# Performance work log

Hardware: AMD Instinct MI355X
Metric: run time of the kernel (lower is better)

## Reference

```python
import jax, jax.numpy as jnp
import numpy as np

B, N, H, K = 2, 4096, 256, 24
IN_DIM = 2 * H + 3  # hidden*2 + 3*num_frames


def setup_inputs() -> dict:
    key = jax.random.key(0)
    ks = jax.random.split(key, 8)
    return {
        "p": jax.random.normal(ks[0], (B, N, 3), jnp.float32),
        "R": jax.random.normal(ks[1], (B, N, 3, 3), jnp.float32),
        "h": jax.random.normal(ks[2], (B, N, H), jnp.float32),
        "W1": jax.random.normal(ks[3], (IN_DIM, H), jnp.float32) * (1.0 / np.sqrt(IN_DIM)),
        "b1": jnp.zeros((H,), jnp.float32),
        "W2": jax.random.normal(ks[4], (H, H), jnp.float32) * (1.0 / np.sqrt(H)),
        "b2": jnp.zeros((H,), jnp.float32),
        "W3": jax.random.normal(ks[5], (H, H), jnp.float32) * (1.0 / np.sqrt(H)),
        "b3": jnp.zeros((H,), jnp.float32),
    }


def _knn_idx(x, k):
    # squared euclidean distances (B,N,N); nearest-k (includes self), like knn_points
    sq = jnp.sum(x * x, axis=-1)
    d = sq[:, :, None] + sq[:, None, :] - 2.0 * jnp.einsum("bnd,bmd->bnm", x, x)
    _, idx = jax.lax.top_k(-d, k)  # (B,N,K)
    return idx


def _gather(x, idx):
    # x: (B,N,D), idx: (B,N,K) -> (B,N,K,D)
    return jax.vmap(lambda a, i: a[i])(x, idx)


def reference(p, R, h, W1, b1, W2, b2, W3, b3):
    leaky = lambda x: jax.nn.leaky_relu(x, 0.1)
    idx = _knn_idx(h, K)                     # graph_type='hidden'
    p_j = _gather(p, idx)                    # (B,N,K,3)
    diff = p_j - p[:, :, None, :]            # global offset
    p_ij = jnp.einsum("bnji,bnkj->bnki", R, diff)  # local frame: R^T (p_j - p_i)
    h_j = _gather(h, idx)                    # (B,N,K,H)
    h_i = jnp.broadcast_to(h[:, :, None, :], h_j.shape)
    feat = jnp.concatenate([p_ij, h_i, h_j], axis=-1)  # (B,N,K,515)
    x = leaky(feat @ W1 + b1)
    x = leaky(x @ W2 + b2)
    x = x @ W3 + b3                          # (B,N,K,H)
    return jnp.max(x, axis=2)                # aggr='max' -> (B,N,H)
```

## Files before the change

### kernel.cpp

```cpp
#include <hip/hip_runtime.h>
#include <stdint.h>

#define BATCH 2
#define NPTS  4096
#define HDIM  256
#define KNN   24
#define NEDGE (BATCH * NPTS * KNN)
#define CAP   256
#define TGT   40

typedef __attribute__((ext_vector_type(8))) short bf16x8;
typedef __attribute__((ext_vector_type(4))) float f32x4;

__device__ __forceinline__ unsigned short f2bf(float f) {
  union { float f; unsigned int u; } x; x.f = f;
  unsigned int u = x.u;
  unsigned int r = (u + 0x7fffu + ((u >> 16) & 1u)) >> 16;
  return (unsigned short)r;
}

__device__ __forceinline__ void gl2lds16(const void* g, void* l) {
  __builtin_amdgcn_global_load_lds(
      (const __attribute__((address_space(1))) unsigned int*)g,
      (__attribute__((address_space(3))) unsigned int*)l, 16, 0, 0);
}

__global__ __launch_bounds__(256) void k_sqnorm(const float* __restrict__ h,
                                                float* __restrict__ sq,
                                                unsigned short* __restrict__ hb) {
  int t = threadIdx.x, lane = t & 63, w = t >> 6;
  int row = blockIdx.x * 4 + w;
  const float* hr = h + (size_t)row * HDIM;
  float4 v = *(const float4*)(hr + lane * 4);
  ushort4 o;
  o.x = f2bf(v.x); o.y = f2bf(v.y); o.z = f2bf(v.z); o.w = f2bf(v.w);
  *(ushort4*)(hb + (size_t)row * HDIM + lane * 4) = o;
  float s = v.x * v.x + v.y * v.y + v.z * v.z + v.w * v.w;
#pragma unroll
  for (int off = 32; off; off >>= 1) s += __shfl_down(s, off);
  if (lane == 0) sq[row] = s;
}

__global__ __launch_bounds__(256) void k_convw(const float* __restrict__ W2,
                                               const float* __restrict__ W3,
                                               unsigned short* __restrict__ w2bt,
                                               unsigned short* __restrict__ w3bt) {
  int t = blockIdx.x * 256 + threadIdx.x;
  int k = t >> 8, n = t & 255;
  w2bt[n * 256 + k] = f2bf(W2[t]);
  w3bt[n * 256 + k] = f2bf(W3[t]);
}

__global__ __launch_bounds__(256) void k_dist(const unsigned short* __restrict__ hb,
                                              const float* __restrict__ sq,
                                              float* __restrict__ D) {
  __shared__ unsigned short At[128 * 32];
  __shared__ unsigned short Bl[128 * 32];
  int b = blockIdx.z;
  int i0 = blockIdx.y * 128, j0 = blockIdx.x * 128;
  const unsigned short* A = hb + (size_t)b * NPTS * HDIM;
  int t = threadIdx.x, lane = t & 63, w = t >> 6;
  int wm = w >> 1, wn = w & 1;
  int lr = lane & 15, lk = (lane >> 4) * 8;
  f32x4 acc[4][4];
#pragma unroll
  for (int i = 0; i < 4; ++i)
#pragma unroll
    for (int j = 0; j < 4; ++j) acc[i][j] = (f32x4){0.f, 0.f, 0.f, 0.f};

  for (int k0 = 0; k0 < HDIM; k0 += 32) {
#pragma unroll
    for (int c = 0; c < 2; ++c) {
      int o = c * 256 + t;
      int row = o >> 2, cb = (o & 3) * 16;
      gl2lds16((const char*)A + ((size_t)(i0 + row) * HDIM + k0) * 2 + cb, (char*)At + o * 16);
      gl2lds16((const char*)A + ((size_t)(j0 + row) * HDIM + k0) * 2 + cb, (char*)Bl + o * 16);
    }
    __syncthreads();
    bf16x8 af[4], bfr[4];
#pragma unroll
    for (int i = 0; i < 4; ++i) af[i] = *(const bf16x8*)&At[(wm * 64 + i * 16 + lr) * 32 + lk];
#pragma unroll
    for (int j = 0; j < 4; ++j) bfr[j] = *(const bf16x8*)&Bl[(wn * 64 + j * 16 + lr) * 32 + lk];
#pragma unroll
    for (int i = 0; i < 4; ++i)
#pragma unroll
      for (int j = 0; j < 4; ++j)
        acc[i][j] = __builtin_amdgcn_mfma_f32_16x16x32_bf16(af[i], bfr[j], acc[i][j], 0, 0, 0);
    __syncthreads();
  }
#pragma unroll
  for (int i = 0; i < 4; ++i)
#pragma unroll
    for (int j = 0; j < 4; ++j)
#pragma unroll
      for (int r = 0; r < 4; ++r) {
        int gi = i0 + wm * 64 + i * 16 + (lane >> 4) * 4 + r;
        int gj = j0 + wn * 64 + j * 16 + lr;
        D[((size_t)b * NPTS + gi) * NPTS + gj] = sq[b * NPTS + gj] - 2.f * acc[i][j][r];
      }
}

__global__ __launch_bounds__(256) void k_topk(const float* __restrict__ D,
                                              const float* __restrict__ h,
                                              int* __restrict__ idxout) {
  int bn = blockIdx.x;
  int b = bn >> 12;
  int t = threadIdx.x, lane = t & 63, w = t >> 6;
  const float* row = D + (size_t)bn * NPTS;

  __shared__ unsigned int hist[2048];
  __shared__ unsigned int h2[256];
  __shared__ int s_ci[CAP];
  __shared__ double s_dv[CAP];
  __shared__ unsigned int s_cnt;
  __shared__ unsigned int s_B;
  __shared__ unsigned int s_cb;
  __shared__ unsigned int s_ub;

  unsigned int key[16];
#pragma unroll
  for (int i = 0; i < 16; ++i) {
    union { float f; unsigned u; } x; x.f = row[i * 256 + t];
    unsigned u = x.u;
    key[i] = u ^ ((unsigned)((int)u >> 31) | 0x80000000u);
  }
  for (int i = t; i < 2048; i += 256) hist[i] = 0;
  if (t == 0) s_cnt = 0;
  __syncthreads();
#pragma unroll
  for (int i = 0; i < 16; ++i) atomicAdd(&hist[key[i] >> 21], 1u);
  __syncthreads();

  if (w == 0) {
    unsigned s = 0;
    int base = lane * 32;
#pragma unroll
    for (int i = 0; i < 32; ++i) s += hist[base + i];
    unsigned ps = s;
    for (int off = 1; off < 64; off <<= 1) {
      unsigned o = __shfl_up(ps, off);
      if (lane >= off) ps += o;
    }
    unsigned before = ps - s;
    bool qual = (ps >= TGT) && (before < TGT);
    unsigned long long mask = __ballot(qual);
    int src = __ffsll((unsigned long long)mask) - 1;
    if (lane == src) {
      unsigned cum = before;
      int B = base;
      for (int i = 0; i < 32; ++i) {
        unsigned c = hist[base + i];
        if (cum + c >= TGT) { B = base + i; break; }
        cum += c;
      }
      s_B = (unsigned)B; s_cb = cum;
    }
  }
  __syncthreads();
  unsigned B = s_B, cb = s_cb;

  if (t < 256) h2[t] = 0;
  __syncthreads();
#pragma unroll
  for (int i = 0; i < 16; ++i)
    if ((key[i] >> 21) == B) atomicAdd(&h2[(key[i] >> 13) & 255u], 1u);
  __syncthreads();
  if (t == 0) {
    unsigned cum = cb;
    int S = 255;
    for (int i = 0; i < 256; ++i) {
      cum += h2[i];
      if (cum >= TGT) { S = i; break; }
    }
    s_ub = (B << 21) + ((unsigned)(S + 1) << 13);
  }
  __syncthreads();
  unsigned ub = s_ub;

#pragma unroll
  for (int i = 0; i < 16; ++i)
    if (key[i] < ub) {
      unsigned pos = atomicAdd(&s_cnt, 1u);
      if (pos < CAP) s_ci[pos] = i * 256 + t;
    }
  __syncthreads();
  int n = (int)s_cnt; if (n > CAP) n = CAP;

  const float* hb = h + (size_t)b * NPTS * HDIM;
  const float* hn = hb + (size_t)(bn & 4095) * HDIM;
  float4 a = *(const float4*)(hn + lane * 4);
  for (int c = w; c < n; c += 4) {
    const float* hm = hb + (size_t)s_ci[c] * HDIM;
    float4 bv = *(const float4*)(hm + lane * 4);
    double d0 = (double)a.x - (double)bv.x;
    double d1 = (double)a.y - (double)bv.y;
    double d2 = (double)a.z - (double)bv.z;
    double d3 = (double)a.w - (double)bv.w;
    double d = d0 * d0 + d1 * d1 + d2 * d2 + d3 * d3;
#pragma unroll
    for (int off = 32; off; off >>= 1) d += __shfl_down(d, off);
    if (lane == 0) s_dv[c] = d;
  }
  __syncthreads();

  for (int c = t; c < n; c += 256) {
    double dc = s_dv[c]; int ic = s_ci[c];
    int rank = 0;
    for (int o = 0; o < n; ++o) {
      double dv = s_dv[o]; int io = s_ci[o];
      if (dv < dc || (dv == dc && io < ic)) ++rank;
    }
    if (rank < KNN) idxout[(size_t)bn * KNN + rank] = ic;
  }
}

__global__ __launch_bounds__(256) void k_nodefeat(const float* __restrict__ h,
                                                  const float* __restrict__ W1,
                                                  const float* __restrict__ b1,
                                                  float* __restrict__ C) {
  int ct = blockIdx.x;
  int i0 = blockIdx.y * 128;
  int wrow = (ct < 2) ? 3 : 259;
  int t = threadIdx.x, tx = t & 15, ty = t >> 4;
  __shared__ float TA[128][17];
  __shared__ float TB[16][128];
  float acc[8][8];
#pragma unroll
  for (int i = 0; i < 8; ++i)
#pragma unroll
    for (int j = 0; j < 8; ++j) acc[i][j] = 0.f;
  int srow = t >> 1, sc = (t & 1) * 8;
  int brow = t >> 4, bc = (t & 15) * 8;

  for (int k0 = 0; k0 < HDIM; k0 += 16) {
    const float* pa = &h[(size_t)(i0 + srow) * HDIM + k0 + sc];
    float4 a0 = *(const float4*)pa, a1 = *(const float4*)(pa + 4);
    const float* pb = &W1[(size_t)(wrow + k0 + brow) * HDIM + (ct & 1) * 128 + bc];
    float4 b0 = *(const float4*)pb, b1v = *(const float4*)(pb + 4);
    __syncthreads();
    TA[srow][sc + 0] = a0.x; TA[srow][sc + 1] = a0.y; TA[srow][sc + 2] = a0.z; TA[srow][sc + 3] = a0.w;
    TA[srow][sc + 4] = a1.x; TA[srow][sc + 5] = a1.y; TA[srow][sc + 6] = a1.z; TA[srow][sc + 7] = a1.w;
    *(float4*)&TB[brow][bc] = b0;
    *(float4*)&TB[brow][bc + 4] = b1v;
    __syncthreads();
#pragma unroll
    for (int kk = 0; kk < 16; ++kk) {
      float av[8], bv[8];
#pragma unroll
      for (int i = 0; i < 8; ++i) av[i] = TA[ty + 16 * i][kk];
#pragma unroll
      for (int j = 0; j < 8; ++j) bv[j] = TB[kk][tx + 16 * j];
#pragma unroll
      for (int i = 0; i < 8; ++i)
#pragma unroll
        for (int j = 0; j < 8; ++j) acc[i][j] += av[i] * bv[j];
    }
  }
#pragma unroll
  for (int i = 0; i < 8; ++i) {
    int gi = i0 + ty + 16 * i;
#pragma unroll
    for (int j = 0; j < 8; ++j) {
      int gc = ct * 128 + tx + 16 * j;
      float vv = acc[i][j];
      if (gc < 256) vv += b1[gc];
      C[(size_t)gi * 512 + gc] = vv;
    }
  }
}

__global__ __launch_bounds__(256) void k_edge1(const float* __restrict__ p,
                                               const float* __restrict__ R,
                                               const float* __restrict__ W1,
                                               const float* __restrict__ C,
                                               const int* __restrict__ idx,
                                               unsigned short* __restrict__ x1) {
  int bn = blockIdx.x;
  int b = bn >> 12;
  int t = threadIdx.x;
  __shared__ int   s_j[KNN];
  __shared__ float s_diff[KNN][3];
  __shared__ float s_pij[KNN][3];
  if (t < KNN) s_j[t] = idx[(size_t)bn * KNN + t];
  __syncthreads();
  if (t < KNN * 3) {
    int k = t / 3, d = t % 3;
    int j = s_j[k];
    s_diff[k][d] = p[((size_t)(b << 12) + j) * 3 + d] - p[(size_t)bn * 3 + d];
  }
  __syncthreads();
  if (t < KNN * 3) {
    int k = t / 3, i = t % 3;
    const float* Rp = R + (size_t)bn * 9;
    s_pij[k][i] = Rp[i] * s_diff[k][0] + Rp[3 + i] * s_diff[k][1] + Rp[6 + i] * s_diff[k][2];
  }
  __syncthreads();
  float w0 = W1[t], w1 = W1[256 + t], w2 = W1[512 + t];
  float a = C[(size_t)bn * 512 + t];
  for (int k = 0; k < KNN; ++k) {
    int j = s_j[k];
    float vv = a + C[((size_t)(b << 12) + j) * 512 + 256 + t]
             + s_pij[k][0] * w0 + s_pij[k][1] * w1 + s_pij[k][2] * w2;
    vv = vv >= 0.f ? vv : 0.1f * vv;
    x1[((size_t)bn * KNN + k) * HDIM + t] = f2bf(vv);
  }
}

__global__ __launch_bounds__(256) void k_gemm2(const unsigned short* __restrict__ A,
                                               const unsigned short* __restrict__ Bt,
                                               const float* __restrict__ bias,
                                               unsigned short* __restrict__ Out) {
  __shared__ unsigned short At[128 * 32];
  __shared__ unsigned short Bl[128 * 32];
  int t = threadIdx.x, lane = t & 63, w = t >> 6;
  int wm = w >> 1, wn = w & 1;
  int m0 = blockIdx.x * 128, n0 = blockIdx.y * 128;
  int lr = lane & 15, lk = (lane >> 4) * 8;
  f32x4 acc[4][4];
#pragma unroll
  for (int i = 0; i < 4; ++i)
#pragma unroll
    for (int j = 0; j < 4; ++j) acc[i][j] = (f32x4){0.f, 0.f, 0.f, 0.f};

  for (int k0 = 0; k0 < 256; k0 += 32) {
#pragma unroll
    for (int c = 0; c < 2; ++c) {
      int o = c * 256 + t;
      int row = o >> 2, cb = (o & 3) * 16;
      gl2lds16((const char*)A + ((size_t)(m0 + row) * 256 + k0) * 2 + cb, (char*)At + o * 16);
      gl2lds16((const char*)Bt + ((size_t)(n0 + row) * 256 + k0) * 2 + cb, (char*)Bl + o * 16);
    }
    __syncthreads();
    bf16x8 af[4], bfr[4];
#pragma unroll
    for (int i = 0; i < 4; ++i) af[i] = *(const bf16x8*)&At[(wm * 64 + i * 16 + lr) * 32 + lk];
#pragma unroll
    for (int j = 0; j < 4; ++j) bfr[j] = *(const bf16x8*)&Bl[(wn * 64 + j * 16 + lr) * 32 + lk];
#pragma unroll
    for (int i = 0; i < 4; ++i)
#pragma unroll
      for (int j = 0; j < 4; ++j)
        acc[i][j] = __builtin_amdgcn_mfma_f32_16x16x32_bf16(af[i], bfr[j], acc[i][j], 0, 0, 0);
    __syncthreads();
  }
#pragma unroll
  for (int i = 0; i < 4; ++i)
#pragma unroll
    for (int j = 0; j < 4; ++j)
#pragma unroll
      for (int r = 0; r < 4; ++r) {
        int grow = m0 + wm * 64 + i * 16 + (lane >> 4) * 4 + r;
        int gcol = n0 + wn * 64 + j * 16 + lr;
        float vv = acc[i][j][r] + bias[gcol];
        vv = vv >= 0.f ? vv : 0.1f * vv;
        Out[(size_t)grow * 256 + gcol] = f2bf(vv);
      }
}

__global__ __launch_bounds__(256) void k_gemm3max(const unsigned short* __restrict__ A,
                                                  const unsigned short* __restrict__ Bt,
                                                  const float* __restrict__ b3,
                                                  float* __restrict__ out) {
  __shared__ float Cs[128 * 129];
  unsigned short* At = (unsigned short*)Cs;
  unsigned short* Bl = At + 128 * 32;
  int t = threadIdx.x, lane = t & 63, w = t >> 6;
  int wm = w >> 1, wn = w & 1;
  int g0 = blockIdx.x * 5;
  int m0 = blockIdx.x * 120;
  int n0 = blockIdx.y * 128;
  int lr = lane & 15, lk = (lane >> 4) * 8;
  f32x4 acc[4][4];
#pragma unroll
  for (int i = 0; i < 4; ++i)
#pragma unroll
    for (int j = 0; j < 4; ++j) acc[i][j] = (f32x4){0.f, 0.f, 0.f, 0.f};

  for (int k0 = 0; k0 < 256; k0 += 32) {
#pragma unroll
    for (int c = 0; c < 2; ++c) {
      int o = c * 256 + t;
      int row = o >> 2, cb = (o & 3) * 16;
      int ar = m0 + row;
      if (ar > NEDGE - 1) ar = NEDGE - 1;
      gl2lds16((const char*)A + ((size_t)ar * 256 + k0) * 2 + cb, (char*)At + o * 16);
      gl2lds16((const char*)Bt + ((size_t)(n0 + row) * 256 + k0) * 2 + cb, (char*)Bl + o * 16);
    }
    __syncthreads();
    bf16x8 af[4], bfr[4];
#pragma unroll
    for (int i = 0; i < 4; ++i) af[i] = *(const bf16x8*)&At[(wm * 64 + i * 16 + lr) * 32 + lk];
#pragma unroll
    for (int j = 0; j < 4; ++j) bfr[j] = *(const bf16x8*)&Bl[(wn * 64 + j * 16 + lr) * 32 + lk];
#pragma unroll
    for (int i = 0; i < 4; ++i)
#pragma unroll
      for (int j = 0; j < 4; ++j)
        acc[i][j] = __builtin_amdgcn_mfma_f32_16x16x32_bf16(af[i], bfr[j], acc[i][j], 0, 0, 0);
    __syncthreads();
  }
#pragma unroll
  for (int i = 0; i < 4; ++i)
#pragma unroll
    for (int j = 0; j < 4; ++j)
#pragma unroll
      for (int r = 0; r < 4; ++r)
        Cs[(wm * 64 + i * 16 + (lane >> 4) * 4 + r) * 129 + wn * 64 + j * 16 + lr] = acc[i][j][r];
  __syncthreads();
  for (int o = t; o < 5 * 128; o += 256) {
    int g = o >> 7, col = o & 127;
    int gg = g0 + g;
    if (gg < BATCH * NPTS) {
      float mx = -3.0e38f;
#pragma unroll
      for (int r = 0; r < KNN; ++r) mx = fmaxf(mx, Cs[(g * 24 + r) * 129 + col]);
      int gcol = n0 + col;
      out[(size_t)gg * 256 + gcol] = mx + b3[gcol];
    }
  }
}

extern "C" void kernel_launch(void* const* d_in, const int* in_sizes, int n_in,
                              void* d_out, int out_size, void* d_ws, size_t ws_size,
                              hipStream_t stream) {
  const float* p  = (const float*)d_in[0];
  const float* R  = (const float*)d_in[1];
  const float* h  = (const float*)d_in[2];
  const float* W1 = (const float*)d_in[3];
  const float* b1 = (const float*)d_in[4];
  const float* W2 = (const float*)d_in[5];
  const float* b2 = (const float*)d_in[6];
  const float* W3 = (const float*)d_in[7];
  const float* b3 = (const float*)d_in[8];
  float* out = (float*)d_out;
  char* ws = (char*)d_ws;

  float*          sq   = (float*)(ws + 0);
  int*            idx  = (int*)(ws + 32768);
  float*          C    = (float*)(ws + 819200);
  unsigned short* w2bt = (unsigned short*)(ws + 17596416);
  unsigned short* w3bt = (unsigned short*)(ws + 17727488);
  char* big = ws + 17858560;
  unsigned short* x1 = (unsigned short*)big;
  unsigned short* x2 = (unsigned short*)(big + 100663296);
  float*          D  = (float*)big;
  unsigned short* hbb = (unsigned short*)(big + 134217728);

  k_sqnorm  <<<dim3(2048),     dim3(256), 0, stream>>>(h, sq, hbb);
  k_convw   <<<dim3(256),      dim3(256), 0, stream>>>(W2, W3, w2bt, w3bt);
  k_dist    <<<dim3(32, 32, 2),dim3(256), 0, stream>>>(hbb, sq, D);
  k_topk    <<<dim3(8192),     dim3(256), 0, stream>>>(D, h, idx);
  k_nodefeat<<<dim3(4, 64),    dim3(256), 0, stream>>>(h, W1, b1, C);
  k_edge1   <<<dim3(8192),     dim3(256), 0, stream>>>(p, R, W1, C, idx, x1);
  k_gemm2   <<<dim3(1536, 2),  dim3(256), 0, stream>>>(x1, w2bt, b2, x2);
  k_gemm3max<<<dim3(1639, 2),  dim3(256), 0, stream>>>(x2, w3bt, b3, out);
}
```

Before: 390.4 us.

## Store distance matrix as 16-bit sortable keys and run top-k one row per wave

The distance kernel now writes the top 16 bits of an order-preserving key instead of full fp32 distances, which halves the traffic for the B*N*N matrix. Top-k selection is restructured so that each wave handles one row on its own, using two 256-bin histogram passes over the 16-bit key and no block-level barriers. The candidate target and cap are retuned (TGT 48, CAP 128). Because candidates are still re-ranked with exact double distances, correctness only depends on the 16-bit threshold keeping enough candidates, and the coarser key risks more ties near the boundary overflowing the smaller cap.

```diff
diff --git a/kernel.cpp b/kernel.cpp
--- a/kernel.cpp
+++ b/kernel.cpp
@@ -6,11 +6,12 @@
 #define HDIM  256
 #define KNN   24
 #define NEDGE (BATCH * NPTS * KNN)
-#define CAP   256
-#define TGT   40
+#define CAP   128
+#define TGT   48
 
 typedef __attribute__((ext_vector_type(8))) short bf16x8;
 typedef __attribute__((ext_vector_type(4))) float f32x4;
+typedef __attribute__((ext_vector_type(8))) unsigned short u16x8;
 
 __device__ __forceinline__ unsigned short f2bf(float f) {
   union { float f; unsigned int u; } x; x.f = f;
@@ -53,7 +54,7 @@
 
 __global__ __launch_bounds__(256) void k_dist(const unsigned short* __restrict__ hb,
                                               const float* __restrict__ sq,
-                                              float* __restrict__ D) {
+                                              unsigned short* __restrict__ D16) {
   __shared__ unsigned short At[128 * 32];
   __shared__ unsigned short Bl[128 * 32];
   int b = blockIdx.z;
@@ -97,101 +98,118 @@
       for (int r = 0; r < 4; ++r) {
         int gi = i0 + wm * 64 + i * 16 + (lane >> 4) * 4 + r;
         int gj = j0 + wn * 64 + j * 16 + lr;
-        D[((size_t)b * NPTS + gi) * NPTS + gj] = sq[b * NPTS + gj] - 2.f * acc[i][j][r];
+        union { float f; unsigned u; } x;
+        x.f = sq[b * NPTS + gj] - 2.f * acc[i][j][r];
+        unsigned m = x.u ^ ((unsigned)((int)x.u >> 31) | 0x80000000u);
+        D16[((size_t)b * NPTS + gi) * NPTS + gj] = (unsigned short)(m >> 16);
       }
 }
 
-__global__ __launch_bounds__(256) void k_topk(const float* __restrict__ D,
+__global__ __launch_bounds__(256) void k_topk(const unsigned short* __restrict__ D16,
                                               const float* __restrict__ h,
                                               int* __restrict__ idxout) {
-  int bn = blockIdx.x;
+  int w = threadIdx.x >> 6, lane = threadIdx.x & 63;
+  int bn = blockIdx.x * 4 + w;
   int b = bn >> 12;
-  int t = threadIdx.x, lane = t & 63, w = t >> 6;
-  const float* row = D + (size_t)bn * NPTS;
-
-  __shared__ unsigned int hist[2048];
-  __shared__ unsigned int h2[256];
-  __shared__ int s_ci[CAP];
-  __shared__ double s_dv[CAP];
-  __shared__ unsigned int s_cnt;
-  __shared__ unsigned int s_B;
-  __shared__ unsigned int s_cb;
-  __shared__ unsigned int s_ub;
-
-  unsigned int key[16];
-#pragma unroll
-  for (int i = 0; i < 16; ++i) {
-    union { float f; unsigned u; } x; x.f = row[i * 256 + t];
-    unsigned u = x.u;
-    key[i] = u ^ ((unsigned)((int)u >> 31) | 0x80000000u);
-  }
-  for (int i = t; i < 2048; i += 256) hist[i] = 0;
-  if (t == 0) s_cnt = 0;
-  __syncthreads();
-#pragma unroll
-  for (int i = 0; i < 16; ++i) atomicAdd(&hist[key[i] >> 21], 1u);
-  __syncthreads();
-
-  if (w == 0) {
-    unsigned s = 0;
-    int base = lane * 32;
-#pragma unroll
-    for (int i = 0; i < 32; ++i) s += hist[base + i];
-    unsigned ps = s;
-    for (int off = 1; off < 64; off <<= 1) {
-      unsigned o = __shfl_up(ps, off);
-      if (lane >= off) ps += o;
-    }
-    unsigned before = ps - s;
-    bool qual = (ps >= TGT) && (before < TGT);
-    unsigned long long mask = __ballot(qual);
-    int src = __ffsll((unsigned long long)mask) - 1;
-    if (lane == src) {
-      unsigned cum = before;
-      int B = base;
-      for (int i = 0; i < 32; ++i) {
-        unsigned c = hist[base + i];
-        if (cum + c >= TGT) { B = base + i; break; }
-        cum += c;
+  const u16x8* rowv = (const u16x8*)(D16 + (size_t)bn * NPTS);
+
+  __shared__ unsigned int hist[4][256];
+  __shared__ int s_ci[4][CAP];
+  __shared__ double s_dv[4][CAP];
+  __shared__ unsigned int s_cnt[4];
+
+  unsigned int* H = hist[w];
+  if (lane == 0) s_cnt[w] = 0;
+
+  u16x8 kv[8];
+#pragma unroll
+  for (int c = 0; c < 8; ++c) kv[c] = rowv[c * 64 + lane];
+
+#pragma unroll
+  for (int i = 0; i < 4; ++i) H[lane * 4 + i] = 0;
+#pragma unroll
+  for (int c = 0; c < 8; ++c)
+#pragma unroll
+    for (int j = 0; j < 8; ++j) atomicAdd(&H[kv[c][j] >> 8], 1u);
+
+  unsigned s = H[lane * 4] + H[lane * 4 + 1] + H[lane * 4 + 2] + H[lane * 4 + 3];
+  unsigned ps = s;
+#pragma unroll
+  for (int off = 1; off < 64; off <<= 1) {
+    unsigned o = __shfl_up(ps, off);
+    if (lane >= off) ps += o;
+  }
+  unsigned before = ps - s;
+  bool qual = (ps >= TGT) && (before < TGT);
+  unsigned long long mask = __ballot(qual);
+  int src = __ffsll(mask) - 1;
+  unsigned B = 0, cb = 0;
+  if (lane == src) {
+    unsigned cum = before;
+    int bb = lane * 4;
+#pragma unroll
+    for (int i = 0; i < 4; ++i) {
+      unsigned c = H[lane * 4 + i];
+      if (cum + c >= TGT) { bb = lane * 4 + i; break; }
+      cum += c;
+    }
+    B = (unsigned)bb; cb = cum;
+  }
+  B = __shfl(B, src); cb = __shfl(cb, src);
+
+#pragma unroll
+  for (int i = 0; i < 4; ++i) H[lane * 4 + i] = 0;
+#pragma unroll
+  for (int c = 0; c < 8; ++c)
+#pragma unroll
+    for (int j = 0; j < 8; ++j) {
+      unsigned k = kv[c][j];
+      if ((k >> 8) == B) atomicAdd(&H[k & 255u], 1u);
+    }
+  unsigned s2 = H[lane * 4] + H[lane * 4 + 1] + H[lane * 4 + 2] + H[lane * 4 + 3];
+  unsigned ps2 = s2;
+#pragma unroll
+  for (int off = 1; off < 64; off <<= 1) {
+    unsigned o = __shfl_up(ps2, off);
+    if (lane >= off) ps2 += o;
+  }
+  unsigned before2 = ps2 - s2;
+  qual = (cb + ps2 >= TGT) && (cb + before2 < TGT);
+  mask = __ballot(qual);
+  src = __ffsll(mask) - 1;
+  unsigned S = 0;
+  if (lane == src) {
+    unsigned cum = cb + before2;
+    int ss = lane * 4;
+#pragma unroll
+    for (int i = 0; i < 4; ++i) {
+      unsigned c = H[lane * 4 + i];
+      if (cum + c >= TGT) { ss = lane * 4 + i; break; }
+      cum += c;
+    }
+    S = (unsigned)ss;
+  }
+  S = __shfl(S, src);
+  unsigned ub = (B << 8) + S + 1;
+
+#pragma unroll
+  for (int c = 0; c < 8; ++c)
+#pragma unroll
+    for (int j = 0; j < 8; ++j) {
+      unsigned k = kv[c][j];
+      if (k < ub) {
+        unsigned pos = atomicAdd(&s_cnt[w], 1u);
+        if (pos < CAP) s_ci[w][pos] = c * 512 + lane * 8 + j;
       }
-      s_B = (unsigned)B; s_cb = cum;
-    }
-  }
-  __syncthreads();
-  unsigned B = s_B, cb = s_cb;
-
-  if (t < 256) h2[t] = 0;
-  __syncthreads();
-#pragma unroll
-  for (int i = 0; i < 16; ++i)
-    if ((key[i] >> 21) == B) atomicAdd(&h2[(key[i] >> 13) & 255u], 1u);
-  __syncthreads();
-  if (t == 0) {
-    unsigned cum = cb;
-    int S = 255;
-    for (int i = 0; i < 256; ++i) {
-      cum += h2[i];
-      if (cum >= TGT) { S = i; break; }
-    }
-    s_ub = (B << 21) + ((unsigned)(S + 1) << 13);
-  }
-  __syncthreads();
-  unsigned ub = s_ub;
-
-#pragma unroll
-  for (int i = 0; i < 16; ++i)
-    if (key[i] < ub) {
-      unsigned pos = atomicAdd(&s_cnt, 1u);
-      if (pos < CAP) s_ci[pos] = i * 256 + t;
-    }
-  __syncthreads();
-  int n = (int)s_cnt; if (n > CAP) n = CAP;
-
-  const float* hb = h + (size_t)b * NPTS * HDIM;
-  const float* hn = hb + (size_t)(bn & 4095) * HDIM;
+    }
+  int n = (int)s_cnt[w];
+  if (n > CAP) n = CAP;
+
+  const float* hbase = h + (size_t)b * NPTS * HDIM;
+  const float* hn = hbase + (size_t)(bn & 4095) * HDIM;
   float4 a = *(const float4*)(hn + lane * 4);
-  for (int c = w; c < n; c += 4) {
-    const float* hm = hb + (size_t)s_ci[c] * HDIM;
+  for (int c = 0; c < n; ++c) {
+    const float* hm = hbase + (size_t)s_ci[w][c] * HDIM;
     float4 bv = *(const float4*)(hm + lane * 4);
     double d0 = (double)a.x - (double)bv.x;
     double d1 = (double)a.y - (double)bv.y;
@@ -200,15 +218,16 @@
     double d = d0 * d0 + d1 * d1 + d2 * d2 + d3 * d3;
 #pragma unroll
     for (int off = 32; off; off >>= 1) d += __shfl_down(d, off);
-    if (lane == 0) s_dv[c] = d;
-  }
-  __syncthreads();
-
-  for (int c = t; c < n; c += 256) {
-    double dc = s_dv[c]; int ic = s_ci[c];
+    if (lane == 0) s_dv[w][c] = d;
+  }
+
+  for (int c = lane; c < n; c += 64) {
+    double dc = s_dv[w][c];
+    int ic = s_ci[w][c];
     int rank = 0;
     for (int o = 0; o < n; ++o) {
-      double dv = s_dv[o]; int io = s_ci[o];
+      double dv = s_dv[w][o];
+      int io = s_ci[w][o];
       if (dv < dc || (dv == dc && io < ic)) ++rank;
     }
     if (rank < KNN) idxout[(size_t)bn * KNN + rank] = ic;
@@ -442,15 +461,15 @@
   unsigned short* w2bt = (unsigned short*)(ws + 17596416);
   unsigned short* w3bt = (unsigned short*)(ws + 17727488);
   char* big = ws + 17858560;
-  unsigned short* x1 = (unsigned short*)big;
-  unsigned short* x2 = (unsigned short*)(big + 100663296);
-  float*          D  = (float*)big;
+  unsigned short* x1  = (unsigned short*)big;
+  unsigned short* x2  = (unsigned short*)(big + 100663296);
+  unsigned short* D16 = (unsigned short*)big;
   unsigned short* hbb = (unsigned short*)(big + 134217728);
 
   k_sqnorm  <<<dim3(2048),     dim3(256), 0, stream>>>(h, sq, hbb);
   k_convw   <<<dim3(256),      dim3(256), 0, stream>>>(W2, W3, w2bt, w3bt);
-  k_dist    <<<dim3(32, 32, 2),dim3(256), 0, stream>>>(hbb, sq, D);
-  k_topk    <<<dim3(8192),     dim3(256), 0, stream>>>(D, h, idx);
+  k_dist    <<<dim3(32, 32, 2),dim3(256), 0, stream>>>(hbb, sq, D16);
+  k_topk    <<<dim3(2048),     dim3(256), 0, stream>>>(D16, h, idx);
   k_nodefeat<<<dim3(4, 64),    dim3(256), 0, stream>>>(h, W1, b1, C);
   k_edge1   <<<dim3(8192),     dim3(256), 0, stream>>>(p, R, W1, C, idx, x1);
   k_gemm2   <<<dim3(1536, 2),  dim3(256), 0, stream>>>(x1, w2bt, b2, x2);
```

Result: slower. 433.8 us (+11.1%).
